# Optimization experiments

Measured on AMD Instinct MI355X. Metric: run time of the kernel, lower is better.

## Reference

```python
import jax, jax.numpy as jnp
import numpy as np

T, D, E, INTER, TOP_K = 512, 1024, 64, 512, 4


def setup_inputs() -> dict:
    key = jax.random.key(0)
    k1, k2, k3, k4, k5 = jax.random.split(key, 5)
    s = 1.0 / np.sqrt(D)
    return {
        "hidden_states": jax.random.normal(k1, (T, D), dtype=jnp.float32),
        "gate_w": jax.random.normal(k2, (E, D), dtype=jnp.float32) * s,      # MoEGate.weight
        "w_gate": jax.random.normal(k3, (E, INTER, D), dtype=jnp.float32) * s,  # gate_proj per expert
        "w_up": jax.random.normal(k4, (E, INTER, D), dtype=jnp.float32) * s,    # up_proj per expert
        "w_down": jax.random.normal(k5, (E, D, INTER), dtype=jnp.float32) * (1.0 / np.sqrt(INTER)),  # down_proj
    }


def _moe_forward(x, gate_w, w_gate, w_up, w_down):
    # Router: logits -> softmax -> top-k -> renormalize (Qwen path of select_experts)
    logits = x @ gate_w.T                                  # [T, E]
    probs = jax.nn.softmax(logits, axis=-1)
    topk_w, topk_ids = jax.lax.top_k(probs, TOP_K)          # [T, K]
    topk_w = topk_w / jnp.sum(topk_w, axis=-1, keepdims=True)  # renormalize (norm_topk_prob)
    # Combine weights as sparse [T, E] matrix (identity logical->physical mapping)
    t_idx = jnp.arange(x.shape[0])[:, None]
    combine = jnp.zeros((x.shape[0], gate_w.shape[0]), dtype=x.dtype).at[t_idx, topk_ids].add(topk_w)
    # Expert FFN (SwiGLU), dense-over-experts reference for grouped GEMM dispatch
    g = jnp.einsum("td,efd->etf", x, w_gate)               # [E, T, INTER]
    u = jnp.einsum("td,efd->etf", x, w_up)
    h = jax.nn.silu(g) * u
    y = jnp.einsum("etf,edf->etd", h, w_down)              # [E, T, D]
    out = jnp.einsum("te,etd->td", combine, y)             # weighted combine
    return out


def reference(hidden_states, gate_w, w_gate, w_up, w_down):
    return _moe_forward(hidden_states, gate_w, w_gate, w_up, w_down)
```

## Files before the change

kernel.cpp:

```cpp
#include <hip/hip_runtime.h>
#include <hip/hip_bf16.h>
#include <cstddef>

#define T_TOK 512
#define D_DIM 1024
#define E_EXP 64
#define INTER 512
#define TOPK 4

__global__ __launch_bounds__(64) void router_kernel(
    const float* __restrict__ x, const float* __restrict__ gate_w,
    int* __restrict__ cnt, int* __restrict__ list, float* __restrict__ pairw) {
  const int t = blockIdx.x;
  const int e = threadIdx.x;
  const float4* xr = (const float4*)(x + (size_t)t * D_DIM);
  const float4* gr = (const float4*)(gate_w + (size_t)e * D_DIM);
  float acc = 0.f;
#pragma unroll 8
  for (int i = 0; i < D_DIM / 4; i++) {
    float4 a = xr[i], b = gr[i];
    acc += a.x * b.x + a.y * b.y + a.z * b.z + a.w * b.w;
  }
  float m = acc;
  for (int off = 32; off; off >>= 1) m = fmaxf(m, __shfl_xor(m, off, 64));
  float p = __expf(acc - m);
  float s = p;
  for (int off = 32; off; off >>= 1) s += __shfl_xor(s, off, 64);
  float prob = p / s;

  float val = prob;
  int ids[TOPK];
  float ws[TOPK];
  float wsum = 0.f;
#pragma unroll
  for (int k = 0; k < TOPK; k++) {
    float v = val;
    int idx = e;
    for (int off = 32; off; off >>= 1) {
      float ov = __shfl_xor(v, off, 64);
      int oi = __shfl_xor(idx, off, 64);
      if (ov > v || (ov == v && oi < idx)) { v = ov; idx = oi; }
    }
    ids[k] = idx;
    ws[k] = v;
    wsum += v;
    if (e == idx) val = -1.f;
  }
  if (e < TOPK) {
    const int k = e;
    const int ex = ids[k];
    const float w = ws[k] / wsum;
    const int p_id = t * TOPK + k;
    pairw[p_id] = w;
    const int pos = atomicAdd(&cnt[ex], 1);
    list[ex * T_TOK + pos] = p_id;
  }
}

#define BF1 32
#define BT1 32
#define BK1 64
#define LD1 (BK1 + 4)
__global__ __launch_bounds__(128) void stage1_kernel(
    const float* __restrict__ x, const float* __restrict__ w_gate,
    const float* __restrict__ w_up, const int* __restrict__ cnt,
    const int* __restrict__ list, const float* __restrict__ pairw,
    float* __restrict__ h) {
  const int e = blockIdx.x;
  const int fbase = blockIdx.y * BF1;
  const int n = cnt[e];
  if (n == 0) return;
  __shared__ float wg[BF1][LD1];
  __shared__ float wu[BF1][LD1];
  __shared__ float xt[BT1][LD1];
  const int tid = threadIdx.x;
  const int f0 = tid & 7;
  const int t0 = tid >> 3;
  const float* Wg = w_gate + ((size_t)e * INTER + fbase) * D_DIM;
  const float* Wu = w_up + ((size_t)e * INTER + fbase) * D_DIM;
  const int* mylist = list + e * T_TOK;

  for (int tb = 0; tb < n; tb += BT1) {
    float accg[4][2], accu[4][2];
#pragma unroll
    for (int i = 0; i < 4; i++)
#pragma unroll
      for (int j = 0; j < 2; j++) { accg[i][j] = 0.f; accu[i][j] = 0.f; }

    for (int kb = 0; kb < D_DIM; kb += BK1) {
#pragma unroll
      for (int r = 0; r < 4; r++) {
        const int idx = tid + 128 * r;
        const int row = idx >> 4;
        const int c4 = (idx & 15) << 2;
        float4 vg = *(const float4*)(Wg + (size_t)row * D_DIM + kb + c4);
        float4 vu = *(const float4*)(Wu + (size_t)row * D_DIM + kb + c4);
        *(float4*)&wg[row][c4] = vg;
        *(float4*)&wu[row][c4] = vu;
      }
#pragma unroll
      for (int r = 0; r < 4; r++) {
        const int idx = tid + 128 * r;
        const int row = idx >> 4;
        const int c4 = (idx & 15) << 2;
        const int slot = tb + row;
        const int pid = mylist[slot < n ? slot : 0];
        const int tok = pid >> 2;
        *(float4*)&xt[row][c4] = *(const float4*)(x + (size_t)tok * D_DIM + kb + c4);
      }
      __syncthreads();
#pragma unroll
      for (int k4 = 0; k4 < BK1; k4 += 4) {
        float4 wgv[4], wuv[4], xv[2];
#pragma unroll
        for (int i = 0; i < 4; i++) {
          wgv[i] = *(const float4*)&wg[f0 + 8 * i][k4];
          wuv[i] = *(const float4*)&wu[f0 + 8 * i][k4];
        }
#pragma unroll
        for (int j = 0; j < 2; j++) xv[j] = *(const float4*)&xt[t0 + 16 * j][k4];
#pragma unroll
        for (int kk = 0; kk < 4; kk++) {
#pragma unroll
          for (int i = 0; i < 4; i++) {
            const float a = ((const float*)&wgv[i])[kk];
            const float b = ((const float*)&wuv[i])[kk];
#pragma unroll
            for (int j = 0; j < 2; j++) {
              const float xx = ((const float*)&xv[j])[kk];
              accg[i][j] += a * xx;
              accu[i][j] += b * xx;
            }
          }
        }
      }
      __syncthreads();
    }
#pragma unroll
    for (int j = 0; j < 2; j++) {
      const int slot = tb + t0 + 16 * j;
      if (slot < n) {
        const int pid = mylist[slot];
        const float wp = pairw[pid];
        float* hp = h + (size_t)pid * INTER + fbase;
#pragma unroll
        for (int i = 0; i < 4; i++) {
          const float g = accg[i][j];
          const float u = accu[i][j];
          const float sg = g / (1.f + __expf(-g));
          hp[f0 + 8 * i] = wp * sg * u;
        }
      }
    }
  }
}

#define BF2 64
#define BT2 32
#define BK2 64
#define LD2 (BK2 + 4)
__global__ __launch_bounds__(128) void stage2_kernel(
    const float* __restrict__ w_down, const int* __restrict__ cnt,
    const int* __restrict__ list, const float* __restrict__ h,
    float* __restrict__ out) {
  const int e = blockIdx.x;
  const int dbase = blockIdx.y * BF2;
  const int n = cnt[e];
  if (n == 0) return;
  __shared__ float wd[BF2][LD2];
  __shared__ float ht[BT2][LD2];
  const int tid = threadIdx.x;
  const int d0 = tid & 15;
  const int t0 = tid >> 4;
  const float* Wd = w_down + ((size_t)e * D_DIM + dbase) * INTER;
  const int* mylist = list + e * T_TOK;

  for (int tb = 0; tb < n; tb += BT2) {
    float acc[4][4];
#pragma unroll
    for (int i = 0; i < 4; i++)
#pragma unroll
      for (int j = 0; j < 4; j++) acc[i][j] = 0.f;

    for (int kb = 0; kb < INTER; kb += BK2) {
#pragma unroll
      for (int r = 0; r < 8; r++) {
        const int idx = tid + 128 * r;
        const int row = idx >> 4;
        const int c4 = (idx & 15) << 2;
        float4 v = *(const float4*)(Wd + (size_t)row * INTER + kb + c4);
        *(float4*)&wd[row][c4] = v;
      }
#pragma unroll
      for (int r = 0; r < 4; r++) {
        const int idx = tid + 128 * r;
        const int row = idx >> 4;
        const int c4 = (idx & 15) << 2;
        const int slot = tb + row;
        const int pid = mylist[slot < n ? slot : 0];
        *(float4*)&ht[row][c4] = *(const float4*)(h + (size_t)pid * INTER + kb + c4);
      }
      __syncthreads();
#pragma unroll
      for (int k4 = 0; k4 < BK2; k4 += 4) {
        float4 wv[4], hv[4];
#pragma unroll
        for (int i = 0; i < 4; i++) wv[i] = *(const float4*)&wd[d0 + 16 * i][k4];
#pragma unroll
        for (int j = 0; j < 4; j++) hv[j] = *(const float4*)&ht[t0 + 8 * j][k4];
#pragma unroll
        for (int kk = 0; kk < 4; kk++) {
#pragma unroll
          for (int i = 0; i < 4; i++) {
            const float a = ((const float*)&wv[i])[kk];
#pragma unroll
            for (int j = 0; j < 4; j++) {
              acc[i][j] += a * ((const float*)&hv[j])[kk];
            }
          }
        }
      }
      __syncthreads();
    }
#pragma unroll
    for (int j = 0; j < 4; j++) {
      const int slot = tb + t0 + 8 * j;
      if (slot < n) {
        const int tok = mylist[slot] >> 2;
        float* op = out + (size_t)tok * D_DIM + dbase;
#pragma unroll
        for (int i = 0; i < 4; i++) {
          atomicAdd(&op[d0 + 16 * i], acc[i][j]);
        }
      }
    }
  }
}

extern "C" void kernel_launch(void* const* d_in, const int* in_sizes, int n_in,
                              void* d_out, int out_size, void* d_ws, size_t ws_size,
                              hipStream_t stream) {
  const float* x = (const float*)d_in[0];
  const float* gate_w = (const float*)d_in[1];
  const float* w_gate = (const float*)d_in[2];
  const float* w_up = (const float*)d_in[3];
  const float* w_down = (const float*)d_in[4];
  float* out = (float*)d_out;

  char* ws = (char*)d_ws;
  int* cnt = (int*)ws;
  int* list = (int*)(ws + 256);
  float* pairw = (float*)(ws + 256 + E_EXP * T_TOK * 4);
  float* h = (float*)(ws + 256 + E_EXP * T_TOK * 4 + T_TOK * TOPK * 4);

  hipMemsetAsync(cnt, 0, E_EXP * sizeof(int), stream);
  hipMemsetAsync(out, 0, (size_t)T_TOK * D_DIM * sizeof(float), stream);

  router_kernel<<<T_TOK, 64, 0, stream>>>(x, gate_w, cnt, list, pairw);
  stage1_kernel<<<dim3(E_EXP, INTER / BF1), 128, 0, stream>>>(
      x, w_gate, w_up, cnt, list, pairw, h);
  stage2_kernel<<<dim3(E_EXP, D_DIM / BF2), 128, 0, stream>>>(
      w_down, cnt, list, h, out);
}
```

Measured before the change: 539.8 us.

## Double token tile and register-prefetch next K slice in both expert GEMMs

After: 686.7 us. 1.27x slower.

```diff
diff --git a/kernel.cpp b/kernel.cpp
--- a/kernel.cpp
+++ b/kernel.cpp
@@ -58,7 +58,7 @@
 }
 
 #define BF1 32
-#define BT1 32
+#define BT1 64
 #define BK1 64
 #define LD1 (BK1 + 4)
 __global__ __launch_bounds__(128) void stage1_kernel(
@@ -79,46 +79,62 @@
   const float* Wg = w_gate + ((size_t)e * INTER + fbase) * D_DIM;
   const float* Wu = w_up + ((size_t)e * INTER + fbase) * D_DIM;
   const int* mylist = list + e * T_TOK;
+  const int srow = tid >> 4;
+  const int sc4 = (tid & 15) << 2;
 
   for (int tb = 0; tb < n; tb += BT1) {
-    float accg[4][2], accu[4][2];
+    const float* xrow[8];
+#pragma unroll
+    for (int r = 0; r < 8; r++) {
+      const int slot = tb + srow + 8 * r;
+      const int pid = mylist[slot < n ? slot : 0];
+      xrow[r] = x + (size_t)(pid >> 2) * D_DIM + sc4;
+    }
+    float accg[4][4], accu[4][4];
 #pragma unroll
     for (int i = 0; i < 4; i++)
 #pragma unroll
-      for (int j = 0; j < 2; j++) { accg[i][j] = 0.f; accu[i][j] = 0.f; }
+      for (int j = 0; j < 4; j++) { accg[i][j] = 0.f; accu[i][j] = 0.f; }
+
+    float4 pg[4], pu[4], px[8];
+#pragma unroll
+    for (int r = 0; r < 4; r++) {
+      pg[r] = *(const float4*)(Wg + (size_t)(srow + 8 * r) * D_DIM + sc4);
+      pu[r] = *(const float4*)(Wu + (size_t)(srow + 8 * r) * D_DIM + sc4);
+    }
+#pragma unroll
+    for (int r = 0; r < 8; r++) px[r] = *(const float4*)xrow[r];
 
     for (int kb = 0; kb < D_DIM; kb += BK1) {
+      if (kb) __syncthreads();
 #pragma unroll
       for (int r = 0; r < 4; r++) {
-        const int idx = tid + 128 * r;
-        const int row = idx >> 4;
-        const int c4 = (idx & 15) << 2;
-        float4 vg = *(const float4*)(Wg + (size_t)row * D_DIM + kb + c4);
-        float4 vu = *(const float4*)(Wu + (size_t)row * D_DIM + kb + c4);
-        *(float4*)&wg[row][c4] = vg;
-        *(float4*)&wu[row][c4] = vu;
-      }
-#pragma unroll
-      for (int r = 0; r < 4; r++) {
-        const int idx = tid + 128 * r;
-        const int row = idx >> 4;
-        const int c4 = (idx & 15) << 2;
-        const int slot = tb + row;
-        const int pid = mylist[slot < n ? slot : 0];
-        const int tok = pid >> 2;
-        *(float4*)&xt[row][c4] = *(const float4*)(x + (size_t)tok * D_DIM + kb + c4);
-      }
+        *(float4*)&wg[srow + 8 * r][sc4] = pg[r];
+        *(float4*)&wu[srow + 8 * r][sc4] = pu[r];
+      }
+#pragma unroll
+      for (int r = 0; r < 8; r++) *(float4*)&xt[srow + 8 * r][sc4] = px[r];
       __syncthreads();
+      if (kb + BK1 < D_DIM) {
+        const int k2 = kb + BK1;
+#pragma unroll
+        for (int r = 0; r < 4; r++) {
+          pg[r] = *(const float4*)(Wg + (size_t)(srow + 8 * r) * D_DIM + k2 + sc4);
+          pu[r] = *(const float4*)(Wu + (size_t)(srow + 8 * r) * D_DIM + k2 + sc4);
+        }
+#pragma unroll
+        for (int r = 0; r < 8; r++) px[r] = *(const float4*)(xrow[r] + k2);
+      }
 #pragma unroll
       for (int k4 = 0; k4 < BK1; k4 += 4) {
-        float4 wgv[4], wuv[4], xv[2];
+        float4 wgv[4], wuv[4], xv[4];
 #pragma unroll
         for (int i = 0; i < 4; i++) {
           wgv[i] = *(const float4*)&wg[f0 + 8 * i][k4];
           wuv[i] = *(const float4*)&wu[f0 + 8 * i][k4];
         }
 #pragma unroll
-        for (int j = 0; j < 2; j++) xv[j] = *(const float4*)&xt[t0 + 16 * j][k4];
+        for (int j = 0; j < 4; j++) xv[j] = *(const float4*)&xt[t0 + 16 * j][k4];
 #pragma unroll
         for (int kk = 0; kk < 4; kk++) {
 #pragma unroll
@@ -126,7 +142,7 @@
             const float a = ((const float*)&wgv[i])[kk];
             const float b = ((const float*)&wuv[i])[kk];
 #pragma unroll
-            for (int j = 0; j < 2; j++) {
+            for (int j = 0; j < 4; j++) {
               const float xx = ((const float*)&xv[j])[kk];
               accg[i][j] += a * xx;
               accu[i][j] += b * xx;
@@ -134,10 +150,9 @@
           }
         }
       }
-      __syncthreads();
-    }
-#pragma unroll
-    for (int j = 0; j < 2; j++) {
+    }
+#pragma unroll
+    for (int j = 0; j < 4; j++) {
       const int slot = tb + t0 + 16 * j;
       if (slot < n) {
         const int pid = mylist[slot];
@@ -152,11 +167,12 @@
         }
       }
     }
+    if (tb + BT1 < n) __syncthreads();
   }
 }
 
 #define BF2 64
-#define BT2 32
+#define BT2 64
 #define BK2 64
 #define LD2 (BK2 + 4)
 __global__ __launch_bounds__(128) void stage2_kernel(
@@ -174,56 +190,68 @@
   const int t0 = tid >> 4;
   const float* Wd = w_down + ((size_t)e * D_DIM + dbase) * INTER;
   const int* mylist = list + e * T_TOK;
+  const int srow = tid >> 4;
+  const int sc4 = (tid & 15) << 2;
 
   for (int tb = 0; tb < n; tb += BT2) {
-    float acc[4][4];
+    const float* hrow[8];
+#pragma unroll
+    for (int r = 0; r < 8; r++) {
+      const int slot = tb + srow + 8 * r;
+      const int pid = mylist[slot < n ? slot : 0];
+      hrow[r] = h + (size_t)pid * INTER + sc4;
+    }
+    float acc[4][8];
 #pragma unroll
     for (int i = 0; i < 4; i++)
 #pragma unroll
-      for (int j = 0; j < 4; j++) acc[i][j] = 0.f;
+      for (int j = 0; j < 8; j++) acc[i][j] = 0.f;
+
+    float4 pw[8], ph[8];
+#pragma unroll
+    for (int r = 0; r < 8; r++) {
+      pw[r] = *(const float4*)(Wd + (size_t)(srow + 8 * r) * INTER + sc4);
+      ph[r] = *(const float4*)hrow[r];
+    }
 
     for (int kb = 0; kb < INTER; kb += BK2) {
+      if (kb) __syncthreads();
 #pragma unroll
       for (int r = 0; r < 8; r++) {
-        const int idx = tid + 128 * r;
-        const int row = idx >> 4;
-        const int c4 = (idx & 15) << 2;
-        float4 v = *(const float4*)(Wd + (size_t)row * INTER + kb + c4);
-        *(float4*)&wd[row][c4] = v;
-      }
-#pragma unroll
-      for (int r = 0; r < 4; r++) {
-        const int idx = tid + 128 * r;
-        const int row = idx >> 4;
-        const int c4 = (idx & 15) << 2;
-        const int slot = tb + row;
-        const int pid = mylist[slot < n ? slot : 0];
-        *(float4*)&ht[row][c4] = *(const float4*)(h + (size_t)pid * INTER + kb + c4);
+        *(float4*)&wd[srow + 8 * r][sc4] = pw[r];
+        *(float4*)&ht[srow + 8 * r][sc4] = ph[r];
       }
       __syncthreads();
+      if (kb + BK2 < INTER) {
+        const int k2 = kb + BK2;
+#pragma unroll
+        for (int r = 0; r < 8; r++) {
+          pw[r] = *(const float4*)(Wd + (size_t)(srow + 8 * r) * INTER + k2 + sc4);
+          ph[r] = *(const float4*)(hrow[r] + k2);
+        }
+      }
 #pragma unroll
       for (int k4 = 0; k4 < BK2; k4 += 4) {
-        float4 wv[4], hv[4];
+        float4 wv[4], hv[8];
 #pragma unroll
         for (int i = 0; i < 4; i++) wv[i] = *(const float4*)&wd[d0 + 16 * i][k4];
 #pragma unroll
-        for (int j = 0; j < 4; j++) hv[j] = *(const float4*)&ht[t0 + 8 * j][k4];
+        for (int j = 0; j < 8; j++) hv[j] = *(const float4*)&ht[t0 + 8 * j][k4];
 #pragma unroll
         for (int kk = 0; kk < 4; kk++) {
 #pragma unroll
           for (int i = 0; i < 4; i++) {
             const float a = ((const float*)&wv[i])[kk];
 #pragma unroll
-            for (int j = 0; j < 4; j++) {
+            for (int j = 0; j < 8; j++) {
               acc[i][j] += a * ((const float*)&hv[j])[kk];
             }
           }
         }
       }
-      __syncthreads();
-    }
-#pragma unroll
-    for (int j = 0; j < 4; j++) {
+    }
+#pragma unroll
+    for (int j = 0; j < 8; j++) {
       const int slot = tb + t0 + 8 * j;
       if (slot < n) {
         const int tok = mylist[slot] >> 2;
@@ -234,6 +262,7 @@
         }
       }
     }
+    if (tb + BT2 < n) __syncthreads();
   }
 }
 
```

## Double-buffer expert GEMMs with async global-to-LDS loads and swizzled tiles

Applied to the files above, without the earlier changes.

After: 513.7 us. 4.8% less time.

```diff
diff --git a/kernel.cpp b/kernel.cpp
--- a/kernel.cpp
+++ b/kernel.cpp
@@ -7,6 +7,12 @@
 #define E_EXP 64
 #define INTER 512
 #define TOPK 4
+
+__device__ __forceinline__ void async16(float4* ldsdst, const float* g) {
+  __builtin_amdgcn_global_load_lds(
+      (const __attribute__((address_space(1))) void*)g,
+      (__attribute__((address_space(3))) void*)ldsdst, 16, 0, 0);
+}
 
 __global__ __launch_bounds__(64) void router_kernel(
     const float* __restrict__ x, const float* __restrict__ gate_w,
@@ -58,10 +64,9 @@
 }
 
 #define BF1 32
-#define BT1 32
+#define BT1 64
 #define BK1 64
-#define LD1 (BK1 + 4)
-__global__ __launch_bounds__(128) void stage1_kernel(
+__global__ __launch_bounds__(256) void stage1_kernel(
     const float* __restrict__ x, const float* __restrict__ w_gate,
     const float* __restrict__ w_up, const int* __restrict__ cnt,
     const int* __restrict__ list, const float* __restrict__ pairw,
@@ -70,63 +75,88 @@
   const int fbase = blockIdx.y * BF1;
   const int n = cnt[e];
   if (n == 0) return;
-  __shared__ float wg[BF1][LD1];
-  __shared__ float wu[BF1][LD1];
-  __shared__ float xt[BT1][LD1];
+  __shared__ float4 lds[2][2048];
   const int tid = threadIdx.x;
-  const int f0 = tid & 7;
-  const int t0 = tid >> 3;
+  const int w = tid >> 6;
+  const int lane = tid & 63;
+  const int f0 = tid & 15;
+  const int t0 = tid >> 4;
   const float* Wg = w_gate + ((size_t)e * INTER + fbase) * D_DIM;
   const float* Wu = w_up + ((size_t)e * INTER + fbase) * D_DIM;
   const int* mylist = list + e * T_TOK;
 
+  int woff[8];
+#pragma unroll
+  for (int r = 0; r < 8; r++) {
+    const int idx = r * 64 + lane;
+    const int row = idx >> 4;
+    const int col = (idx & 15) ^ (row & 7);
+    woff[r] = row * D_DIM + 4 * col;
+  }
+
   for (int tb = 0; tb < n; tb += BT1) {
-    float accg[4][2], accu[4][2];
-#pragma unroll
-    for (int i = 0; i < 4; i++)
-#pragma unroll
-      for (int j = 0; j < 2; j++) { accg[i][j] = 0.f; accu[i][j] = 0.f; }
-
-    for (int kb = 0; kb < D_DIM; kb += BK1) {
-#pragma unroll
-      for (int r = 0; r < 4; r++) {
-        const int idx = tid + 128 * r;
+    const float* xp[8];
+    if (w >= 2) {
+#pragma unroll
+      for (int r = 0; r < 8; r++) {
+        const int c = (w - 2) * 8 + r;
+        const int idx = c * 64 + lane;
         const int row = idx >> 4;
-        const int c4 = (idx & 15) << 2;
-        float4 vg = *(const float4*)(Wg + (size_t)row * D_DIM + kb + c4);
-        float4 vu = *(const float4*)(Wu + (size_t)row * D_DIM + kb + c4);
-        *(float4*)&wg[row][c4] = vg;
-        *(float4*)&wu[row][c4] = vu;
-      }
-#pragma unroll
-      for (int r = 0; r < 4; r++) {
-        const int idx = tid + 128 * r;
-        const int row = idx >> 4;
-        const int c4 = (idx & 15) << 2;
+        const int col = (idx & 15) ^ (row & 7);
         const int slot = tb + row;
         const int pid = mylist[slot < n ? slot : 0];
-        const int tok = pid >> 2;
-        *(float4*)&xt[row][c4] = *(const float4*)(x + (size_t)tok * D_DIM + kb + c4);
-      }
+        xp[r] = x + (size_t)(pid >> 2) * D_DIM + 4 * col;
+      }
+    }
+    auto stage = [&](int buf, int kb) {
+      float4* B = &lds[buf][0];
+      if (w == 0) {
+#pragma unroll
+        for (int r = 0; r < 8; r++) async16(B + r * 64, Wg + woff[r] + kb);
+      } else if (w == 1) {
+#pragma unroll
+        for (int r = 0; r < 8; r++) async16(B + 512 + r * 64, Wu + woff[r] + kb);
+      } else {
+        const int c0 = (w - 2) * 8;
+#pragma unroll
+        for (int r = 0; r < 8; r++)
+          async16(B + 1024 + (c0 + r) * 64, xp[r] + kb);
+      }
+    };
+
+    float accg[2][4], accu[2][4];
+#pragma unroll
+    for (int i = 0; i < 2; i++)
+#pragma unroll
+      for (int j = 0; j < 4; j++) { accg[i][j] = 0.f; accu[i][j] = 0.f; }
+
+    stage(0, 0);
+    for (int ki = 0; ki < D_DIM / BK1; ki++) {
       __syncthreads();
-#pragma unroll
-      for (int k4 = 0; k4 < BK1; k4 += 4) {
-        float4 wgv[4], wuv[4], xv[2];
-#pragma unroll
-        for (int i = 0; i < 4; i++) {
-          wgv[i] = *(const float4*)&wg[f0 + 8 * i][k4];
-          wuv[i] = *(const float4*)&wu[f0 + 8 * i][k4];
+      if (ki + 1 < D_DIM / BK1) stage((ki + 1) & 1, (ki + 1) * BK1);
+      const float4* wgb = &lds[ki & 1][0];
+      const float4* wub = wgb + 512;
+      const float4* xtb = wgb + 1024;
+#pragma unroll
+      for (int k4 = 0; k4 < 16; k4++) {
+        float4 wgv[2], wuv[2], xv[4];
+#pragma unroll
+        for (int i = 0; i < 2; i++) {
+          const int off = (f0 + 16 * i) * 16 + (k4 ^ (f0 & 7));
+          wgv[i] = wgb[off];
+          wuv[i] = wub[off];
         }
 #pragma unroll
-        for (int j = 0; j < 2; j++) xv[j] = *(const float4*)&xt[t0 + 16 * j][k4];
+        for (int j = 0; j < 4; j++)
+          xv[j] = xtb[(t0 + 16 * j) * 16 + (k4 ^ (t0 & 7))];
 #pragma unroll
         for (int kk = 0; kk < 4; kk++) {
 #pragma unroll
-          for (int i = 0; i < 4; i++) {
+          for (int i = 0; i < 2; i++) {
             const float a = ((const float*)&wgv[i])[kk];
             const float b = ((const float*)&wuv[i])[kk];
 #pragma unroll
-            for (int j = 0; j < 2; j++) {
+            for (int j = 0; j < 4; j++) {
               const float xx = ((const float*)&xv[j])[kk];
               accg[i][j] += a * xx;
               accu[i][j] += b * xx;
@@ -134,21 +164,19 @@
           }
         }
       }
-      __syncthreads();
-    }
-#pragma unroll
-    for (int j = 0; j < 2; j++) {
+    }
+#pragma unroll
+    for (int j = 0; j < 4; j++) {
       const int slot = tb + t0 + 16 * j;
       if (slot < n) {
         const int pid = mylist[slot];
         const float wp = pairw[pid];
         float* hp = h + (size_t)pid * INTER + fbase;
 #pragma unroll
-        for (int i = 0; i < 4; i++) {
+        for (int i = 0; i < 2; i++) {
           const float g = accg[i][j];
           const float u = accu[i][j];
-          const float sg = g / (1.f + __expf(-g));
-          hp[f0 + 8 * i] = wp * sg * u;
+          hp[f0 + 16 * i] = wp * (g / (1.f + __expf(-g))) * u;
         }
       }
     }
@@ -156,10 +184,9 @@
 }
 
 #define BF2 64
-#define BT2 32
+#define BT2 64
 #define BK2 64
-#define LD2 (BK2 + 4)
-__global__ __launch_bounds__(128) void stage2_kernel(
+__global__ __launch_bounds__(256) void stage2_kernel(
     const float* __restrict__ w_down, const int* __restrict__ cnt,
     const int* __restrict__ list, const float* __restrict__ h,
     float* __restrict__ out) {
@@ -167,71 +194,98 @@
   const int dbase = blockIdx.y * BF2;
   const int n = cnt[e];
   if (n == 0) return;
-  __shared__ float wd[BF2][LD2];
-  __shared__ float ht[BT2][LD2];
+  __shared__ float4 lds[2][2048];
   const int tid = threadIdx.x;
+  const int w = tid >> 6;
+  const int lane = tid & 63;
   const int d0 = tid & 15;
   const int t0 = tid >> 4;
   const float* Wd = w_down + ((size_t)e * D_DIM + dbase) * INTER;
   const int* mylist = list + e * T_TOK;
 
+  int woff[8];
+  if (w < 2) {
+#pragma unroll
+    for (int r = 0; r < 8; r++) {
+      const int c = w * 8 + r;
+      const int idx = c * 64 + lane;
+      const int row = idx >> 4;
+      const int col = (idx & 15) ^ (row & 7);
+      woff[r] = row * INTER + 4 * col;
+    }
+  }
+
   for (int tb = 0; tb < n; tb += BT2) {
-    float acc[4][4];
-#pragma unroll
-    for (int i = 0; i < 4; i++)
-#pragma unroll
-      for (int j = 0; j < 4; j++) acc[i][j] = 0.f;
-
-    for (int kb = 0; kb < INTER; kb += BK2) {
+    const float* hp8[8];
+    if (w >= 2) {
 #pragma unroll
       for (int r = 0; r < 8; r++) {
-        const int idx = tid + 128 * r;
+        const int c = (w - 2) * 8 + r;
+        const int idx = c * 64 + lane;
         const int row = idx >> 4;
-        const int c4 = (idx & 15) << 2;
-        float4 v = *(const float4*)(Wd + (size_t)row * INTER + kb + c4);
-        *(float4*)&wd[row][c4] = v;
-      }
-#pragma unroll
-      for (int r = 0; r < 4; r++) {
-        const int idx = tid + 128 * r;
-        const int row = idx >> 4;
-        const int c4 = (idx & 15) << 2;
+        const int col = (idx & 15) ^ (row & 7);
         const int slot = tb + row;
         const int pid = mylist[slot < n ? slot : 0];
-        *(float4*)&ht[row][c4] = *(const float4*)(h + (size_t)pid * INTER + kb + c4);
-      }
+        hp8[r] = h + (size_t)pid * INTER + 4 * col;
+      }
+    }
+    auto stage = [&](int buf, int kb) {
+      float4* B = &lds[buf][0];
+      if (w < 2) {
+        const int c0 = w * 8;
+#pragma unroll
+        for (int r = 0; r < 8; r++)
+          async16(B + (c0 + r) * 64, Wd + woff[r] + kb);
+      } else {
+        const int c0 = (w - 2) * 8;
+#pragma unroll
+        for (int r = 0; r < 8; r++)
+          async16(B + 1024 + (c0 + r) * 64, hp8[r] + kb);
+      }
+    };
+
+    float acc[4][4];
+#pragma unroll
+    for (int i = 0; i < 4; i++)
+#pragma unroll
+      for (int j = 0; j < 4; j++) acc[i][j] = 0.f;
+
+    stage(0, 0);
+    for (int ki = 0; ki < INTER / BK2; ki++) {
       __syncthreads();
-#pragma unroll
-      for (int k4 = 0; k4 < BK2; k4 += 4) {
+      if (ki + 1 < INTER / BK2) stage((ki + 1) & 1, (ki + 1) * BK2);
+      const float4* wdb = &lds[ki & 1][0];
+      const float4* htb = wdb + 1024;
+#pragma unroll
+      for (int k4 = 0; k4 < 16; k4++) {
         float4 wv[4], hv[4];
 #pragma unroll
-        for (int i = 0; i < 4; i++) wv[i] = *(const float4*)&wd[d0 + 16 * i][k4];
-#pragma unroll
-        for (int j = 0; j < 4; j++) hv[j] = *(const float4*)&ht[t0 + 8 * j][k4];
+        for (int i = 0; i < 4; i++)
+          wv[i] = wdb[(d0 + 16 * i) * 16 + (k4 ^ (d0 & 7))];
+#pragma unroll
+        for (int j = 0; j < 4; j++)
+          hv[j] = htb[(t0 + 16 * j) * 16 + (k4 ^ (t0 & 7))];
 #pragma unroll
         for (int kk = 0; kk < 4; kk++) {
 #pragma unroll
           for (int i = 0; i < 4; i++) {
             const float a = ((const float*)&wv[i])[kk];
 #pragma unroll
-            for (int j = 0; j < 4; j++) {
+            for (int j = 0; j < 4; j++)
               acc[i][j] += a * ((const float*)&hv[j])[kk];
-            }
           }
         }
       }
-      __syncthreads();
     }
 #pragma unroll
     for (int j = 0; j < 4; j++) {
-      const int slot = tb + t0 + 8 * j;
+      const int slot = tb + t0 + 16 * j;
       if (slot < n) {
         const int tok = mylist[slot] >> 2;
         float* op = out + (size_t)tok * D_DIM + dbase;
 #pragma unroll
-        for (int i = 0; i < 4; i++) {
+        for (int i = 0; i < 4; i++)
           atomicAdd(&op[d0 + 16 * i], acc[i][j]);
-        }
       }
     }
   }
@@ -257,8 +311,8 @@
   hipMemsetAsync(out, 0, (size_t)T_TOK * D_DIM * sizeof(float), stream);
 
   router_kernel<<<T_TOK, 64, 0, stream>>>(x, gate_w, cnt, list, pairw);
-  stage1_kernel<<<dim3(E_EXP, INTER / BF1), 128, 0, stream>>>(
+  stage1_kernel<<<dim3(E_EXP, INTER / BF1), 256, 0, stream>>>(
       x, w_gate, w_up, cnt, list, pairw, h);
-  stage2_kernel<<<dim3(E_EXP, D_DIM / BF2), 128, 0, stream>>>(
+  stage2_kernel<<<dim3(E_EXP, D_DIM / BF2), 256, 0, stream>>>(
       w_down, cnt, list, h, out);
 }
```
